# Kernel optimization log

Measured on AMD Instinct MI355X. Metric: run time of the kernel, lower is better.

## Reference

```python
import jax, jax.numpy as jnp
import numpy as np

NUM_STATES = 4096
SEQ_LEN = 4096


def setup_inputs() -> dict:
    key = jax.random.key(0)
    k1, k2, k3, k4 = jax.random.split(key, 4)
    state_dist = jax.random.uniform(k1, (NUM_STATES,), dtype=jnp.float32)
    input_seq = jax.random.randint(k2, (SEQ_LEN,), 0, 2, dtype=jnp.int64)
    T = jax.random.normal(k3, (NUM_STATES, 2, NUM_STATES), dtype=jnp.float32) * 0.1
    O = jax.random.normal(k4, (NUM_STATES, 2, 4), dtype=jnp.float32) * 0.1
    return {"state_dist": state_dist, "input_seq": input_seq, "T": T, "O": O}


def reference(state_dist, input_seq, T, O):
    # Softmax over last dim -> row-stochastic transition / emission matrices.
    Tm = jax.nn.softmax(T, axis=-1)  # [N, 2, N]
    Om = jax.nn.softmax(O, axis=-1)  # [N, 2, 4]

    def step(state, sym):
        # (O[:, sym, :] * state[:, None]).sum(0) == state @ O[:, sym, :]
        O_s = jnp.take(Om, sym, axis=1)          # [N, 4]
        T_s = jnp.take(Tm, sym, axis=1)          # [N, N]
        out_prob = state @ O_s                    # [4]
        new_state = state @ T_s                   # [N]
        return new_state, out_prob

    _, outputs = jax.lax.scan(step, state_dist, input_seq)
    return outputs  # [L, 4]
```

## Files before the change

### kernel.cpp

```cpp
#include <hip/hip_runtime.h>
#include <hip/hip_fp16.h>

#define N 4096
#define L 4096
#define NPART 16
#define NJB 32
#define CPB 128
#define RPB 256

#define NN ((size_t)N * (size_t)N)
#define SLOT ((size_t)N * 4)
#define VTN ((size_t)NPART * N)

#define ASU(p, v) __hip_atomic_store((p), (v), __ATOMIC_RELAXED, __HIP_MEMORY_SCOPE_AGENT)
#define ALU(p)    __hip_atomic_load((p), __ATOMIC_RELAXED, __HIP_MEMORY_SCOPE_AGENT)

typedef _Float16 f16x8 __attribute__((ext_vector_type(8)));
typedef float f32x4 __attribute__((ext_vector_type(4)));

__global__ __launch_bounds__(256) void init_kernel(const float* __restrict__ sd,
                                                   unsigned long long* __restrict__ vt,
                                                   float* __restrict__ rcacc,
                                                   float* __restrict__ out) {
    int g = blockIdx.x * 256 + threadIdx.x;
    if (g < L * 4) out[g] = 0.0f;
    if (g < (int)(3 * VTN)) {
        float val = (g < N) ? sd[g] : 0.0f;
        ASU(&vt[g], (unsigned long long)__float_as_uint(val));
    }
    if (g < 16 * N) rcacc[g] = 0.0f;
}

__global__ __launch_bounds__(256) void build_desc_kernel(const int* __restrict__ seq32,
                                                         unsigned char* __restrict__ midx,
                                                         int mode) {
    __shared__ int any_odd;
    if (threadIdx.x == 0) any_odd = 0;
    __syncthreads();
    int acc = 0;
    for (int i = threadIdx.x; i < L / 2; i += 256) acc |= seq32[2 * i + 1];
    if (acc) any_odd = 1;
    __syncthreads();
    const int is64 = (any_odd == 0);
#define SYM(t) ((is64 ? seq32[2 * (t)] : seq32[(t)]) & 1)
    if (mode == 2) {
        for (int k = threadIdx.x; k < L / 4; k += 256)
            midx[k] = (unsigned char)(SYM(4 * k) * 8 + SYM(4 * k + 1) * 4 +
                                      SYM(4 * k + 2) * 2 + SYM(4 * k + 3));
    } else if (mode == 1) {
        for (int k = threadIdx.x; k < L / 2; k += 256)
            midx[k] = (unsigned char)(SYM(2 * k) * 2 + SYM(2 * k + 1));
    } else {
        for (int t = threadIdx.x; t < L; t += 256)
            midx[t] = (unsigned char)SYM(t);
    }
#undef SYM
}

__global__ __launch_bounds__(256) void softmax_T_kernel(const float* __restrict__ T,
                                                        unsigned short* __restrict__ Tm,
                                                        float* __restrict__ rowc) {
    int row = blockIdx.x;
    int i = row >> 1, s = row & 1;
    const float* src = T + (size_t)row * N;
    unsigned short* dst = Tm + ((size_t)s << 24) + ((size_t)i << 12);
    int tid = threadIdx.x;

    float vals[16];
    float mx = -1e30f;
#pragma unroll
    for (int k = 0; k < 16; k++) {
        vals[k] = src[tid + (k << 8)];
        mx = fmaxf(mx, vals[k]);
    }
#pragma unroll
    for (int o = 32; o > 0; o >>= 1) mx = fmaxf(mx, __shfl_xor(mx, o));
    __shared__ float red[4];
    int wid = tid >> 6;
    if ((tid & 63) == 0) red[wid] = mx;
    __syncthreads();
    mx = fmaxf(fmaxf(red[0], red[1]), fmaxf(red[2], red[3]));
    __syncthreads();

    float sum = 0.0f;
#pragma unroll
    for (int k = 0; k < 16; k++) {
        vals[k] = __expf(vals[k] - mx);
        sum += vals[k];
    }
#pragma unroll
    for (int o = 32; o > 0; o >>= 1) sum += __shfl_xor(sum, o);
    if ((tid & 63) == 0) red[wid] = sum;
    __syncthreads();
    sum = red[0] + red[1] + red[2] + red[3];
    __syncthreads();
    float inv = 1.0f / sum;

    float qs = 0.0f;
#pragma unroll
    for (int k = 0; k < 16; k++) {
        __half h = __float2half_rn(vals[k] * inv);
        dst[tid + (k << 8)] = __half_as_ushort(h);
        qs += __half2float(h);
    }
#pragma unroll
    for (int o = 32; o > 0; o >>= 1) qs += __shfl_xor(qs, o);
    if ((tid & 63) == 0) red[wid] = qs;
    __syncthreads();
    if (tid == 0) {
        float q = red[0] + red[1] + red[2] + red[3];
        rowc[(size_t)s * N + i] = 1.0f / q;
    }
}

__global__ __launch_bounds__(256) void softmax_O_kernel(const float* __restrict__ O,
                                                        float* __restrict__ OW) {
    int r = blockIdx.x * 256 + threadIdx.x;
    if (r < 2 * N) {
        float4 x = *(const float4*)(O + (size_t)r * 4);
        float mx = fmaxf(fmaxf(x.x, x.y), fmaxf(x.z, x.w));
        float e0 = __expf(x.x - mx), e1 = __expf(x.y - mx);
        float e2 = __expf(x.z - mx), e3 = __expf(x.w - mx);
        float inv = 1.0f / (e0 + e1 + e2 + e3);
        int i = r >> 1, s = r & 1;
        *(float4*)(OW + (size_t)s * SLOT + (size_t)i * 4) =
            make_float4(e0 * inv, e1 * inv, e2 * inv, e3 * inv);
    }
}

template <int Q8OUT>
__global__ __launch_bounds__(256) void gemm_kernel(const unsigned short* __restrict__ Abase,
                                                   const unsigned short* __restrict__ Bbase,
                                                   void* __restrict__ Cbase,
                                                   float* __restrict__ rcacc,
                                                   int ash, int bmask) {
    int bid = blockIdx.x;
    int pair = bid >> 10;
    int tile = bid & 1023;
    int i0 = (tile >> 5) << 7;
    int j0 = (tile & 31) << 7;
    const unsigned short* A = Abase + (size_t)(pair >> ash) * NN;
    const unsigned short* B = Bbase + (size_t)(pair & bmask) * NN;

    __shared__ _Float16 Asd[128][40];
    __shared__ unsigned int Btw[128][20];

    const int tid = threadIdx.x;
    const int w = tid >> 6, ln = tid & 63;
    const int wrow = (w >> 1) << 6, wcol = (w & 1) << 6;
    const int q = ln >> 4, l15 = ln & 15;

    const int ar = tid >> 1, ah = tid & 1;
    const int bk2 = tid & 15, bng = tid >> 4;

    f32x4 acc[4][4] = {};

    for (int k0 = 0; k0 < N; k0 += 32) {
        const uint4* ga = (const uint4*)(A + (size_t)(i0 + ar) * N + k0 + ah * 16);
        uint4 a0 = ga[0], a1 = ga[1];
        *(uint4*)&Asd[ar][ah * 16] = a0;
        *(uint4*)&Asd[ar][ah * 16 + 8] = a1;
        const unsigned short* gb0 = B + (size_t)(k0 + 2 * bk2) * N + j0 + bng * 8;
        uint4 b0 = *(const uint4*)gb0;
        uint4 b1 = *(const uint4*)(gb0 + N);
        const unsigned short* e0 = (const unsigned short*)&b0;
        const unsigned short* e1 = (const unsigned short*)&b1;
#pragma unroll
        for (int jj = 0; jj < 8; jj++)
            Btw[bng * 8 + jj][bk2] = (unsigned)e0[jj] | ((unsigned)e1[jj] << 16);
        __syncthreads();

        f16x8 af[4], bf[4];
#pragma unroll
        for (int ti = 0; ti < 4; ti++)
            af[ti] = *(const f16x8*)&Asd[wrow + ti * 16 + l15][q * 8];
#pragma unroll
        for (int tj = 0; tj < 4; tj++)
            bf[tj] = *(const f16x8*)&Btw[wcol + tj * 16 + l15][q * 4];
#pragma unroll
        for (int ti = 0; ti < 4; ti++)
#pragma unroll
            for (int tj = 0; tj < 4; tj++)
                acc[ti][tj] = __builtin_amdgcn_mfma_f32_16x16x32_f16(
                    af[ti], bf[tj], acc[ti][tj], 0, 0, 0);
        __syncthreads();
    }

    if (Q8OUT == 0) {
        unsigned short* Pm = (unsigned short*)Cbase + (size_t)pair * NN;
#pragma unroll
        for (int ti = 0; ti < 4; ti++)
#pragma unroll
            for (int tj = 0; tj < 4; tj++)
#pragma unroll
                for (int reg = 0; reg < 4; reg++) {
                    int row = i0 + wrow + ti * 16 + q * 4 + reg;
                    int col = j0 + wcol + tj * 16 + l15;
                    Pm[(size_t)row * N + col] =
                        __half_as_ushort(__float2half_rn(acc[ti][tj][reg]));
                }
    } else {
        unsigned char* Pm8 = (unsigned char*)Cbase + (size_t)pair * NN;
        float* rcrow = rcacc + (size_t)pair * N;
#pragma unroll
        for (int ti = 0; ti < 4; ti++)
#pragma unroll
            for (int reg = 0; reg < 4; reg++) {
                int row = i0 + wrow + ti * 16 + q * 4 + reg;
                float rs = 0.0f;
#pragma unroll
                for (int tj = 0; tj < 4; tj++) {
                    float f = acc[ti][tj][reg] * 16384.0f;
                    unsigned hb = __half_as_ushort(__float2half_rn(f));
                    unsigned r = hb + 0x3Fu + ((hb >> 7) & 1u);
                    int qv = (int)(r >> 7) - 64;
                    qv = qv < 8 ? 8 : (qv > 0x7E ? 0x7E : qv);
                    unsigned short db = (unsigned short)((qv + 64) << 7);
                    rs += __half2float(*reinterpret_cast<const __half*>(&db));
                    Pm8[(size_t)row * N + j0 + wcol + tj * 16 + l15] = (unsigned char)qv;
                }
                rs += __shfl_xor(rs, 1); rs += __shfl_xor(rs, 2);
                rs += __shfl_xor(rs, 4); rs += __shfl_xor(rs, 8);
                if (l15 == 0) atomicAdd(&rcrow[row], rs);
            }
    }
}

__global__ __launch_bounds__(256) void rcinv_kernel(float* __restrict__ rc) {
    int g = blockIdx.x * 256 + threadIdx.x;
    if (g < 16 * N) rc[g] = 1.0f / rc[g];
}

__global__ __launch_bounds__(256) void rowsum_kernel(const unsigned short* __restrict__ P,
                                                     float* __restrict__ rc) {
    int b = blockIdx.x;
    const unsigned short* row = P + (size_t)b * N;
    int tid = threadIdx.x;
    const uint4* rp = (const uint4*)row + tid * 2;
    uint4 w0 = rp[0], w1 = rp[1];
    const __half* h0 = (const __half*)&w0;
    const __half* h1 = (const __half*)&w1;
    float s = 0.0f;
#pragma unroll
    for (int j = 0; j < 8; j++) s += __half2float(h0[j]) + __half2float(h1[j]);
#pragma unroll
    for (int o = 32; o > 0; o >>= 1) s += __shfl_xor(s, o);
    __shared__ float red[4];
    if ((tid & 63) == 0) red[tid >> 6] = s;
    __syncthreads();
    if (tid == 0) rc[b] = 1.0f / (red[0] + red[1] + red[2] + red[3]);
}

__global__ __launch_bounds__(256) void proj_kernel(const unsigned short* __restrict__ Tm,
                                                   const unsigned short* __restrict__ P,
                                                   const float* __restrict__ rowc,
                                                   const float* __restrict__ rowc2,
                                                   float* __restrict__ OW, int phase) {
    int bid = blockIdx.x;
    int s = bid >> 12, i = bid & 4095;
    const unsigned short* M; const float* rc; const float* Q; float* dst;
    if (phase == 1) {
        if (s < 4) { M = Tm + (size_t)(s >> 1) * NN; rc = rowc + (size_t)(s >> 1) * N;
                     Q = OW + (size_t)(s & 1) * SLOT; dst = OW + (size_t)(2 + s) * SLOT; }
        else { int q = s - 4; M = P + (size_t)(q >> 1) * NN; rc = rowc2 + (size_t)(q >> 1) * N;
               Q = OW + (size_t)(q & 1) * SLOT; dst = OW + (size_t)(6 + q) * SLOT; }
    } else {
        int q = s; M = P + (size_t)(q >> 2) * NN; rc = rowc2 + (size_t)(q >> 2) * N;
        Q = OW + (size_t)(2 + (q & 3)) * SLOT; dst = OW + (size_t)(14 + q) * SLOT;
    }
    const unsigned short* row = M + (size_t)i * N;
    int tid = threadIdx.x;
    const uint4* rp = (const uint4*)row + tid * 2;
    uint4 w0 = rp[0], w1 = rp[1];
    const __half* h0 = (const __half*)&w0;
    const __half* h1 = (const __half*)&w1;
    int j0 = tid * 16;
    float ac[4] = {};
#pragma unroll
    for (int j = 0; j < 8; j++) {
        float tv = __half2float(h0[j]);
        float4 o = *(const float4*)(Q + (size_t)(j0 + j) * 4);
        ac[0] += tv * o.x; ac[1] += tv * o.y; ac[2] += tv * o.z; ac[3] += tv * o.w;
        float tv1 = __half2float(h1[j]);
        float4 o1 = *(const float4*)(Q + (size_t)(j0 + 8 + j) * 4);
        ac[0] += tv1 * o1.x; ac[1] += tv1 * o1.y; ac[2] += tv1 * o1.z; ac[3] += tv1 * o1.w;
    }
#pragma unroll
    for (int e = 0; e < 4; e++)
#pragma unroll
        for (int o = 32; o > 0; o >>= 1) ac[e] += __shfl_xor(ac[e], o);
    __shared__ float red[4][4];
    if ((tid & 63) == 0)
#pragma unroll
        for (int e = 0; e < 4; e++) red[tid >> 6][e] = ac[e];
    __syncthreads();
    if (tid < 4)
        dst[(size_t)i * 4 + tid] =
            (red[0][tid] + red[1][tid] + red[2][tid] + red[3][tid]) * rc[i];
}

__device__ __forceinline__ float2 d8x2(unsigned b0, unsigned b1) {
    unsigned pk = ((b0 + 64u) << 7) | ((b1 + 64u) << 23);
    return __half22float2(*reinterpret_cast<__half2*>(&pk));
}

#define SPIN_SUM(vinp, kk, accv)                                               \
    {                                                                          \
        unsigned long long uv[16];                                             \
        _Pragma("unroll")                                                      \
        for (int p = 0; p < 16; p++) uv[p] = ALU((vinp) + p * N);              \
        unsigned miss = 0;                                                     \
        _Pragma("unroll")                                                      \
        for (int p = 0; p < 16; p++)                                           \
            if ((unsigned)(uv[p] >> 32) != (kk)) miss |= 1u << p;              \
        while (__builtin_expect(miss != 0, 0)) {                               \
            _Pragma("unroll")                                                  \
            for (int p = 0; p < 16; p++)                                       \
                if (miss & (1u << p)) {                                        \
                    unsigned long long t = ALU((vinp) + p * N);                \
                    if ((unsigned)(t >> 32) == (kk)) { uv[p] = t; miss &= ~(1u << p); } \
                }                                                              \
        }                                                                      \
        _Pragma("unroll")                                                      \
        for (int p = 0; p < 16; p++) accv += __uint_as_float((unsigned)uv[p]); \
    }

__global__ __launch_bounds__(256, 2) void scan8_kernel(const unsigned char* __restrict__ Q8,
                                                       const float* __restrict__ rc,
                                                       const float* __restrict__ OW,
                                                       const unsigned char* __restrict__ midx,
                                                       unsigned long long* __restrict__ vt,
                                                       float* __restrict__ out,
                                                       int S, int OPS) {
    const int tid = threadIdx.x;
    const int jb = blockIdx.x & 31;
    const int ic = blockIdx.x >> 5;
    const int i0 = ic * RPB;
    const int j0 = jb * CPB;

    __shared__ unsigned char mt8[2][RPB][CPB];
    __shared__ float v[RPB];
    __shared__ float vc[RPB];
    __shared__ float colacc[CPB];

    const int cg = tid & 15;
    const int rg = tid >> 4;

    const int w4 = tid >> 6;
    const int ln = tid & 63;
    const size_t goff8 = (size_t)(i0 + (ln >> 3)) * N + j0 + (ln & 7) * 16;

#define STAGE8(Mb, dst)                                                         \
    _Pragma("unroll")                                                           \
    for (int t = 0; t < 8; t++) {                                               \
        const int row0 = w4 * 64 + t * 8;                                       \
        __builtin_amdgcn_global_load_lds(                                       \
            (const __attribute__((address_space(1))) unsigned int*)((Mb) + goff8 + (size_t)row0 * N), \
            (__attribute__((address_space(3))) unsigned int*)((dst) + (size_t)row0 * CPB),            \
            16, 0, 0);                                                          \
    }

    int mcur = (int)midx[0];
    int mnxt = (S > 1) ? (int)midx[1] : 0;
    float rc_cur = rc[(size_t)mcur * N + i0 + tid];
    float rc_nxt = (S > 1) ? rc[(size_t)mnxt * N + i0 + tid] : 0.0f;
    STAGE8(Q8 + (size_t)mcur * NN, &mt8[0][0][0]);

    for (int k = 0; k < S; k++) {
        const int m = mcur;
        const unsigned long long* vinp = vt + (size_t)(k % 3) * VTN + (i0 + tid);
        unsigned long long* voutp = vt + (size_t)((k + 1) % 3) * VTN + (size_t)ic * N + j0;
        const unsigned char* mtc = &mt8[k & 1][0][0];

        float accv = 0.0f;
        SPIN_SUM(vinp, (unsigned)k, accv);
        v[tid] = accv;
        vc[tid] = accv * rc_cur;
        if (tid < CPB) colacc[tid] = 0.0f;

        if (k + 1 < S) {
            STAGE8(Q8 + (size_t)mnxt * NN, &mt8[(k + 1) & 1][0][0]);
            asm volatile("s_waitcnt vmcnt(8) lgkmcnt(0)" ::: "memory");
        } else {
            asm volatile("s_waitcnt vmcnt(0) lgkmcnt(0)" ::: "memory");
        }
        __builtin_amdgcn_s_barrier();
        __builtin_amdgcn_sched_barrier(0);

        float a[8];
#pragma unroll
        for (int e = 0; e < 8; e++) a[e] = 0.0f;
#pragma unroll
        for (int r = 0; r < 16; r++) {
            uint2 w = *(const uint2*)(mtc + (size_t)(rg * 16 + r) * CPB + cg * 8);
            float vi = vc[rg * 16 + r];
            float2 f0 = d8x2(w.x & 0xFF, (w.x >> 8) & 0xFF);
            float2 f1 = d8x2((w.x >> 16) & 0xFF, w.x >> 24);
            float2 f2 = d8x2(w.y & 0xFF, (w.y >> 8) & 0xFF);
            float2 f3 = d8x2((w.y >> 16) & 0xFF, w.y >> 24);
            a[0] += vi * f0.x; a[1] += vi * f0.y;
            a[2] += vi * f1.x; a[3] += vi * f1.y;
            a[4] += vi * f2.x; a[5] += vi * f2.y;
            a[6] += vi * f3.x; a[7] += vi * f3.y;
        }
#pragma unroll
        for (int e = 0; e < 8; e++) atomicAdd(&colacc[cg * 8 + e], a[e]);

        if (jb < OPS) {
            int slot;
            if (OPS == 4) slot = (jb == 0) ? (m >> 3) : (jb == 1) ? 2 + (m >> 2)
                               : (jb == 2) ? 6 + (m >> 1) : 14 + m;
            else if (OPS == 2) slot = (jb == 0) ? (m >> 1) : 2 + m;
            else slot = m;
            const float* pr = OW + (size_t)slot * SLOT;
            int r = tid >> 2, c = tid & 3;
            float p = v[r]       * pr[(size_t)(i0 + r) * 4 + c]
                    + v[r + 64]  * pr[(size_t)(i0 + r + 64) * 4 + c]
                    + v[r + 128] * pr[(size_t)(i0 + r + 128) * 4 + c]
                    + v[r + 192] * pr[(size_t)(i0 + r + 192) * 4 + c];
            p += __shfl_down(p, 32); p += __shfl_down(p, 16);
            p += __shfl_down(p, 8);  p += __shfl_down(p, 4);
            if ((tid & 63) < 4) atomicAdd(&out[(k * OPS + jb) * 4 + (tid & 3)], p);
        }

        asm volatile("s_waitcnt lgkmcnt(0)" ::: "memory");
        __builtin_amdgcn_s_barrier();
        __builtin_amdgcn_sched_barrier(0);

        if (tid < CPB) {
            unsigned long long pk = ((unsigned long long)(unsigned)(k + 1) << 32)
                                  | (unsigned long long)__float_as_uint(colacc[tid]);
            ASU(&voutp[tid], pk);
        }
        mcur = mnxt; rc_cur = rc_nxt;
        if (k + 2 < S) {
            mnxt = (int)midx[k + 2];
            rc_nxt = rc[(size_t)mnxt * N + i0 + tid];
        }
    }
#undef STAGE8
}

__global__ __launch_bounds__(256, 2) void scan16_kernel(const unsigned short* __restrict__ Mbase,
                                                        const float* __restrict__ rc,
                                                        const float* __restrict__ OW,
                                                        const unsigned char* __restrict__ midx,
                                                        unsigned long long* __restrict__ vt,
                                                        float* __restrict__ out,
                                                        int S, int OPS) {
    const int tid = threadIdx.x;
    const int jb = blockIdx.x & 31;
    const int ic = blockIdx.x >> 5;
    const int i0 = ic * RPB;
    const int j0 = jb * CPB;

    __shared__ unsigned short mt[RPB][CPB];
    __shared__ float v[RPB];
    __shared__ float vc[RPB];
    __shared__ float colacc[CPB];

    const int cg = tid & 15;
    const int rg = tid >> 4;

    const int w4 = tid >> 6;
    const int ln = tid & 63;
    const size_t goff = (size_t)(i0 + (ln >> 4)) * N + j0 + (ln & 15) * 8;

    int mcur = (int)midx[0];
    int mnxt = (S > 1) ? (int)midx[1] : 0;
    float rc_cur = rc[(size_t)mcur * N + i0 + tid];
    float rc_nxt = (S > 1) ? rc[(size_t)mnxt * N + i0 + tid] : 0.0f;
    {
        const unsigned short* Mb = Mbase + (size_t)mcur * NN;
#pragma unroll
        for (int t = 0; t < 16; t++) {
            const int row0 = w4 * 64 + t * 4;
            __builtin_amdgcn_global_load_lds(
                (const __attribute__((address_space(1))) unsigned int*)(Mb + goff + (size_t)row0 * N),
                (__attribute__((address_space(3))) unsigned int*)(&mt[row0][0]),
                16, 0, 0);
        }
    }

    for (int k = 0; k < S; k++) {
        const int m = mcur;
        const unsigned long long* vinp = vt + (size_t)(k % 3) * VTN + (i0 + tid);
        unsigned long long* voutp = vt + (size_t)((k + 1) % 3) * VTN + (size_t)ic * N + j0;

        float accv = 0.0f;
        SPIN_SUM(vinp, (unsigned)k, accv);
        v[tid] = accv;
        vc[tid] = accv * rc_cur;
        if (tid < CPB) colacc[tid] = 0.0f;
        __syncthreads();

        float a[8];
#pragma unroll
        for (int e = 0; e < 8; e++) a[e] = 0.0f;
#pragma unroll
        for (int r = 0; r < 16; r++) {
            uint4 w = *(const uint4*)&mt[rg * 16 + r][cg * 8];
            float vi = vc[rg * 16 + r];
            float2 f0 = __half22float2(*(__half2*)&w.x);
            float2 f1 = __half22float2(*(__half2*)&w.y);
            float2 f2 = __half22float2(*(__half2*)&w.z);
            float2 f3 = __half22float2(*(__half2*)&w.w);
            a[0] += vi * f0.x; a[1] += vi * f0.y;
            a[2] += vi * f1.x; a[3] += vi * f1.y;
            a[4] += vi * f2.x; a[5] += vi * f2.y;
            a[6] += vi * f3.x; a[7] += vi * f3.y;
        }
#pragma unroll
        for (int e = 0; e < 8; e++) atomicAdd(&colacc[cg * 8 + e], a[e]);

        if (jb < OPS) {
            int slot;
            if (OPS == 4) slot = (jb == 0) ? (m >> 3) : (jb == 1) ? 2 + (m >> 2)
                               : (jb == 2) ? 6 + (m >> 1) : 14 + m;
            else if (OPS == 2) slot = (jb == 0) ? (m >> 1) : 2 + m;
            else slot = m;
            const float* pr = OW + (size_t)slot * SLOT;
            int r = tid >> 2, c = tid & 3;
            float p = v[r]       * pr[(size_t)(i0 + r) * 4 + c]
                    + v[r + 64]  * pr[(size_t)(i0 + r + 64) * 4 + c]
                    + v[r + 128] * pr[(size_t)(i0 + r + 128) * 4 + c]
                    + v[r + 192] * pr[(size_t)(i0 + r + 192) * 4 + c];
            p += __shfl_down(p, 32); p += __shfl_down(p, 16);
            p += __shfl_down(p, 8);  p += __shfl_down(p, 4);
            if ((tid & 63) < 4) atomicAdd(&out[(k * OPS + jb) * 4 + (tid & 3)], p);
        }
        __syncthreads();

        if (tid < CPB) {
            unsigned long long pk = ((unsigned long long)(unsigned)(k + 1) << 32)
                                  | (unsigned long long)__float_as_uint(colacc[tid]);
            ASU(&voutp[tid], pk);
        }
        if (k + 1 < S) {
            const unsigned short* Mb = Mbase + (size_t)mnxt * NN;
#pragma unroll
            for (int t = 0; t < 16; t++) {
                const int row0 = w4 * 64 + t * 4;
                __builtin_amdgcn_global_load_lds(
                    (const __attribute__((address_space(1))) unsigned int*)(Mb + goff + (size_t)row0 * N),
                    (__attribute__((address_space(3))) unsigned int*)(&mt[row0][0]),
                    16, 0, 0);
            }
        }
        mcur = mnxt; rc_cur = rc_nxt;
        if (k + 2 < S) {
            mnxt = (int)midx[k + 2];
            rc_nxt = rc[(size_t)mnxt * N + i0 + tid];
        }
    }
}

extern "C" void kernel_launch(void* const* d_in, const int* in_sizes, int n_in,
                              void* d_out, int out_size, void* d_ws, size_t ws_size,
                              hipStream_t stream) {
    const float* sd  = (const float*)d_in[0];
    const int*   seq = (const int*)d_in[1];
    const float* T   = (const float*)d_in[2];
    const float* O   = (const float*)d_in[3];
    float* out = (float*)d_out;

    const size_t TM_SZ = 2 * NN * 2;
    const size_t P_SZ  = 4 * NN * 2;
    const size_t Q8_SZ = 16 * NN;
    const size_t AUX_SZ = 0x400000;

    int mode = (ws_size >= TM_SZ + P_SZ + Q8_SZ + AUX_SZ) ? 3
             : (ws_size >= TM_SZ + P_SZ + AUX_SZ) ? 1 : 0;

    char* ws = (char*)d_ws;
    unsigned short* Tm = (unsigned short*)ws;
    unsigned short* P  = (unsigned short*)(ws + TM_SZ);
    unsigned char*  Q8 = (unsigned char*)(ws + TM_SZ + P_SZ);
    char* aux = ws + (mode == 3 ? TM_SZ + P_SZ + Q8_SZ
                    : mode == 1 ? TM_SZ + P_SZ : TM_SZ);
    float* rowc   = (float*)(aux);
    float* rowc2  = (float*)(aux + 0x8000);
    float* rowc4  = (float*)(aux + 0x18000);
    float* OW     = (float*)(aux + 0x58000);
    unsigned long long* vt = (unsigned long long*)(aux + 0x258000);
    unsigned char* midx = (unsigned char*)(aux + 0x3D8000);

    hipLaunchKernelGGL(init_kernel, dim3(1536), dim3(256), 0, stream, sd, vt, rowc4, out);
    hipLaunchKernelGGL(build_desc_kernel, dim3(1), dim3(256), 0, stream, seq, midx,
                       mode == 3 ? 2 : mode);
    hipLaunchKernelGGL(softmax_T_kernel, dim3(2 * N), dim3(256), 0, stream, T, Tm, rowc);
    hipLaunchKernelGGL(softmax_O_kernel, dim3(32), dim3(256), 0, stream, O, OW);

    if (mode == 3) {
        hipLaunchKernelGGL(HIP_KERNEL_NAME(gemm_kernel<0>), dim3(4 * 1024), dim3(256), 0, stream,
                           Tm, Tm, (void*)P, rowc4, 1, 1);
        hipLaunchKernelGGL(rowsum_kernel, dim3(4 * N), dim3(256), 0, stream, P, rowc2);
        hipLaunchKernelGGL(HIP_KERNEL_NAME(gemm_kernel<1>), dim3(16 * 1024), dim3(256), 0, stream,
                           P, P, (void*)Q8, rowc4, 2, 3);
        hipLaunchKernelGGL(rcinv_kernel, dim3(256), dim3(256), 0, stream, rowc4);
        hipLaunchKernelGGL(proj_kernel, dim3(12 * N), dim3(256), 0, stream, Tm, P, rowc, rowc2, OW, 1);
        hipLaunchKernelGGL(proj_kernel, dim3(16 * N), dim3(256), 0, stream, Tm, P, rowc, rowc2, OW, 2);
        hipLaunchKernelGGL(scan8_kernel, dim3(512), dim3(256), 0, stream,
                           Q8, rowc4, OW, midx, vt, out, L / 4, 4);
    } else if (mode == 1) {
        hipLaunchKernelGGL(HIP_KERNEL_NAME(gemm_kernel<0>), dim3(4 * 1024), dim3(256), 0, stream,
                           Tm, Tm, (void*)P, rowc4, 1, 1);
        hipLaunchKernelGGL(rowsum_kernel, dim3(4 * N), dim3(256), 0, stream, P, rowc2);
        hipLaunchKernelGGL(proj_kernel, dim3(4 * N), dim3(256), 0, stream, Tm, P, rowc, rowc2, OW, 1);
        hipLaunchKernelGGL(scan16_kernel, dim3(512), dim3(256), 0, stream,
                           P, rowc2, OW, midx, vt, out, L / 2, 2);
    } else {
        hipLaunchKernelGGL(scan16_kernel, dim3(512), dim3(256), 0, stream,
                           Tm, rowc, OW, midx, vt, out, L, 1);
    }
}
```

Measured before the change: 15.18 ms.

## Gate scan steps on per-producer ready flags and publish results earlier

Adds a ready-flag array. Each block publishes a step counter after writing its partial column sums, and consumer blocks wait on the 32 producer flags with sleeping polls before reading the packed vector values. The partial-vector store and flag publish are moved ahead of the output-probability computation, so downstream blocks can start the next step sooner. s_sleep is also added to the miss-retry loop to reduce memory pressure from spinning. The cost is an extra barrier and flag traffic per step, and possible added latency from the sleeps.

```diff
diff --git a/kernel.cpp b/kernel.cpp
--- a/kernel.cpp
+++ b/kernel.cpp
@@ -21,6 +21,7 @@
 __global__ __launch_bounds__(256) void init_kernel(const float* __restrict__ sd,
                                                    unsigned long long* __restrict__ vt,
                                                    float* __restrict__ rcacc,
+                                                   unsigned* __restrict__ ready,
                                                    float* __restrict__ out) {
     int g = blockIdx.x * 256 + threadIdx.x;
     if (g < L * 4) out[g] = 0.0f;
@@ -29,6 +30,7 @@
         ASU(&vt[g], (unsigned long long)__float_as_uint(val));
     }
     if (g < 16 * N) rcacc[g] = 0.0f;
+    if (g < NPART * 64) ASU(&ready[g], 0u);
 }
 
 __global__ __launch_bounds__(256) void build_desc_kernel(const int* __restrict__ seq32,
@@ -314,6 +316,7 @@
         for (int p = 0; p < 16; p++)                                           \
             if ((unsigned)(uv[p] >> 32) != (kk)) miss |= 1u << p;              \
         while (__builtin_expect(miss != 0, 0)) {                               \
+            __builtin_amdgcn_s_sleep(1);                                       \
             _Pragma("unroll")                                                  \
             for (int p = 0; p < 16; p++)                                       \
                 if (miss & (1u << p)) {                                        \
@@ -330,6 +333,7 @@
                                                        const float* __restrict__ OW,
                                                        const unsigned char* __restrict__ midx,
                                                        unsigned long long* __restrict__ vt,
+                                                       unsigned* __restrict__ ready,
                                                        float* __restrict__ out,
                                                        int S, int OPS) {
     const int tid = threadIdx.x;
@@ -349,6 +353,9 @@
     const int w4 = tid >> 6;
     const int ln = tid & 63;
     const size_t goff8 = (size_t)(i0 + (ln >> 3)) * N + j0 + (ln & 7) * 16;
+
+    unsigned* wait_flags = &ready[ic * 64];
+    unsigned* my_flag    = &ready[(jb >> 1) * 64 + ic * 2 + (jb & 1)];
 
 #define STAGE8(Mb, dst)                                                         \
     _Pragma("unroll")                                                           \
@@ -371,6 +378,13 @@
         const unsigned long long* vinp = vt + (size_t)(k % 3) * VTN + (i0 + tid);
         unsigned long long* voutp = vt + (size_t)((k + 1) % 3) * VTN + (size_t)ic * N + j0;
         const unsigned char* mtc = &mt8[k & 1][0][0];
+
+        if (tid < 32) {
+            while (ALU(&wait_flags[tid]) < (unsigned)k) __builtin_amdgcn_s_sleep(2);
+        }
+        asm volatile("" ::: "memory");
+        __builtin_amdgcn_s_barrier();
+        asm volatile("" ::: "memory");
 
         float accv = 0.0f;
         SPIN_SUM(vinp, (unsigned)k, accv);
@@ -405,6 +419,17 @@
         }
 #pragma unroll
         for (int e = 0; e < 8; e++) atomicAdd(&colacc[cg * 8 + e], a[e]);
+
+        asm volatile("s_waitcnt lgkmcnt(0)" ::: "memory");
+        __builtin_amdgcn_s_barrier();
+        __builtin_amdgcn_sched_barrier(0);
+
+        if (tid < CPB) {
+            unsigned long long pk = ((unsigned long long)(unsigned)(k + 1) << 32)
+                                  | (unsigned long long)__float_as_uint(colacc[tid]);
+            ASU(&voutp[tid], pk);
+        }
+        if (tid == 0) ASU(my_flag, (unsigned)(k + 1));
 
         if (jb < OPS) {
             int slot;
@@ -423,15 +448,6 @@
             if ((tid & 63) < 4) atomicAdd(&out[(k * OPS + jb) * 4 + (tid & 3)], p);
         }
 
-        asm volatile("s_waitcnt lgkmcnt(0)" ::: "memory");
-        __builtin_amdgcn_s_barrier();
-        __builtin_amdgcn_sched_barrier(0);
-
-        if (tid < CPB) {
-            unsigned long long pk = ((unsigned long long)(unsigned)(k + 1) << 32)
-                                  | (unsigned long long)__float_as_uint(colacc[tid]);
-            ASU(&voutp[tid], pk);
-        }
         mcur = mnxt; rc_cur = rc_nxt;
         if (k + 2 < S) {
             mnxt = (int)midx[k + 2];
@@ -446,6 +462,7 @@
                                                         const float* __restrict__ OW,
                                                         const unsigned char* __restrict__ midx,
                                                         unsigned long long* __restrict__ vt,
+                                                        unsigned* __restrict__ ready,
                                                         float* __restrict__ out,
                                                         int S, int OPS) {
     const int tid = threadIdx.x;
@@ -466,6 +483,9 @@
     const int ln = tid & 63;
     const size_t goff = (size_t)(i0 + (ln >> 4)) * N + j0 + (ln & 15) * 8;
 
+    unsigned* wait_flags = &ready[ic * 64];
+    unsigned* my_flag    = &ready[(jb >> 1) * 64 + ic * 2 + (jb & 1)];
+
     int mcur = (int)midx[0];
     int mnxt = (S > 1) ? (int)midx[1] : 0;
     float rc_cur = rc[(size_t)mcur * N + i0 + tid];
@@ -486,6 +506,13 @@
         const int m = mcur;
         const unsigned long long* vinp = vt + (size_t)(k % 3) * VTN + (i0 + tid);
         unsigned long long* voutp = vt + (size_t)((k + 1) % 3) * VTN + (size_t)ic * N + j0;
+
+        if (tid < 32) {
+            while (ALU(&wait_flags[tid]) < (unsigned)k) __builtin_amdgcn_s_sleep(2);
+        }
+        asm volatile("" ::: "memory");
+        __builtin_amdgcn_s_barrier();
+        asm volatile("" ::: "memory");
 
         float accv = 0.0f;
         SPIN_SUM(vinp, (unsigned)k, accv);
@@ -512,6 +539,14 @@
         }
 #pragma unroll
         for (int e = 0; e < 8; e++) atomicAdd(&colacc[cg * 8 + e], a[e]);
+        __syncthreads();
+
+        if (tid < CPB) {
+            unsigned long long pk = ((unsigned long long)(unsigned)(k + 1) << 32)
+                                  | (unsigned long long)__float_as_uint(colacc[tid]);
+            ASU(&voutp[tid], pk);
+        }
+        if (tid == 0) ASU(my_flag, (unsigned)(k + 1));
 
         if (jb < OPS) {
             int slot;
@@ -529,13 +564,7 @@
             p += __shfl_down(p, 8);  p += __shfl_down(p, 4);
             if ((tid & 63) < 4) atomicAdd(&out[(k * OPS + jb) * 4 + (tid & 3)], p);
         }
-        __syncthreads();
-
-        if (tid < CPB) {
-            unsigned long long pk = ((unsigned long long)(unsigned)(k + 1) << 32)
-                                  | (unsigned long long)__float_as_uint(colacc[tid]);
-            ASU(&voutp[tid], pk);
-        }
+
         if (k + 1 < S) {
             const unsigned short* Mb = Mbase + (size_t)mnxt * NN;
 #pragma unroll
@@ -584,8 +613,9 @@
     float* OW     = (float*)(aux + 0x58000);
     unsigned long long* vt = (unsigned long long*)(aux + 0x258000);
     unsigned char* midx = (unsigned char*)(aux + 0x3D8000);
-
-    hipLaunchKernelGGL(init_kernel, dim3(1536), dim3(256), 0, stream, sd, vt, rowc4, out);
+    unsigned* ready = (unsigned*)(aux + 0x3D9000);
+
+    hipLaunchKernelGGL(init_kernel, dim3(1536), dim3(256), 0, stream, sd, vt, rowc4, ready, out);
     hipLaunchKernelGGL(build_desc_kernel, dim3(1), dim3(256), 0, stream, seq, midx,
                        mode == 3 ? 2 : mode);
     hipLaunchKernelGGL(softmax_T_kernel, dim3(2 * N), dim3(256), 0, stream, T, Tm, rowc);
@@ -601,16 +631,16 @@
         hipLaunchKernelGGL(proj_kernel, dim3(12 * N), dim3(256), 0, stream, Tm, P, rowc, rowc2, OW, 1);
         hipLaunchKernelGGL(proj_kernel, dim3(16 * N), dim3(256), 0, stream, Tm, P, rowc, rowc2, OW, 2);
         hipLaunchKernelGGL(scan8_kernel, dim3(512), dim3(256), 0, stream,
-                           Q8, rowc4, OW, midx, vt, out, L / 4, 4);
+                           Q8, rowc4, OW, midx, vt, ready, out, L / 4, 4);
     } else if (mode == 1) {
         hipLaunchKernelGGL(HIP_KERNEL_NAME(gemm_kernel<0>), dim3(4 * 1024), dim3(256), 0, stream,
                            Tm, Tm, (void*)P, rowc4, 1, 1);
         hipLaunchKernelGGL(rowsum_kernel, dim3(4 * N), dim3(256), 0, stream, P, rowc2);
         hipLaunchKernelGGL(proj_kernel, dim3(4 * N), dim3(256), 0, stream, Tm, P, rowc, rowc2, OW, 1);
         hipLaunchKernelGGL(scan16_kernel, dim3(512), dim3(256), 0, stream,
-                           P, rowc2, OW, midx, vt, out, L / 2, 2);
+                           P, rowc2, OW, midx, vt, ready, out, L / 2, 2);
     } else {
         hipLaunchKernelGGL(scan16_kernel, dim3(512), dim3(256), 0, stream,
-                           Tm, rowc, OW, midx, vt, out, L, 1);
-    }
-}
+                           Tm, rowc, OW, midx, vt, ready, out, L, 1);
+    }
+}
```

Result: slower. 16.00 ms (+5.4%).

## Use direct global-to-LDS loads with XOR swizzle, K=64 tiles, and XCD-aware block remap

Applied to the files above, without the earlier changes.

The GEMM kernel's K-step doubles from 32 to 64, which halves the number of barriers per tile. The A tile is loaded with global_load_lds straight into an XOR-swizzled shared-memory layout, skipping the round trip through registers and avoiding bank conflicts. Block IDs are remapped so consecutive tiles land on the same XCD, which should improve L2 reuse. In exchange, shared memory use and register pressure both rise.

```diff
diff --git a/kernel.cpp b/kernel.cpp
--- a/kernel.cpp
+++ b/kernel.cpp
@@ -134,7 +134,9 @@
                                                    void* __restrict__ Cbase,
                                                    float* __restrict__ rcacc,
                                                    int ash, int bmask) {
-    int bid = blockIdx.x;
+    const int nwg = gridDim.x;
+    int bid0 = blockIdx.x;
+    int bid = (bid0 & 7) * (nwg >> 3) + (bid0 >> 3);
     int pair = bid >> 10;
     int tile = bid & 1023;
     int i0 = (tile >> 5) << 7;
@@ -142,47 +144,67 @@
     const unsigned short* A = Abase + (size_t)(pair >> ash) * NN;
     const unsigned short* B = Bbase + (size_t)(pair & bmask) * NN;
 
-    __shared__ _Float16 Asd[128][40];
-    __shared__ unsigned int Btw[128][20];
+    __shared__ _Float16 Asd[128 * 64];
+    __shared__ unsigned int Btw[128][36];
 
     const int tid = threadIdx.x;
     const int w = tid >> 6, ln = tid & 63;
     const int wrow = (w >> 1) << 6, wcol = (w & 1) << 6;
     const int q = ln >> 4, l15 = ln & 15;
 
-    const int ar = tid >> 1, ah = tid & 1;
-    const int bk2 = tid & 15, bng = tid >> 4;
+    const int kp = tid & 31, cgB = tid >> 5;
+
+    const int gA = (ln & 7) ^ (ln >> 3);
 
     f32x4 acc[4][4] = {};
 
-    for (int k0 = 0; k0 < N; k0 += 32) {
-        const uint4* ga = (const uint4*)(A + (size_t)(i0 + ar) * N + k0 + ah * 16);
-        uint4 a0 = ga[0], a1 = ga[1];
-        *(uint4*)&Asd[ar][ah * 16] = a0;
-        *(uint4*)&Asd[ar][ah * 16 + 8] = a1;
-        const unsigned short* gb0 = B + (size_t)(k0 + 2 * bk2) * N + j0 + bng * 8;
-        uint4 b0 = *(const uint4*)gb0;
-        uint4 b1 = *(const uint4*)(gb0 + N);
-        const unsigned short* e0 = (const unsigned short*)&b0;
-        const unsigned short* e1 = (const unsigned short*)&b1;
+    for (int k0 = 0; k0 < N; k0 += 64) {
+#pragma unroll
+        for (int t = 0; t < 4; t++) {
+            const int rbase = w * 32 + t * 8;
+            const int r = rbase + (ln >> 3);
+            __builtin_amdgcn_global_load_lds(
+                (const __attribute__((address_space(1))) unsigned int*)
+                    (A + (size_t)(i0 + r) * N + k0 + gA * 8),
+                (__attribute__((address_space(3))) unsigned int*)(Asd + rbase * 64),
+                16, 0, 0);
+        }
+        const unsigned short* gb0 = B + (size_t)(k0 + 2 * kp) * N + j0 + cgB * 16;
+        uint4 b0  = *(const uint4*)gb0;
+        uint4 b0h = *(const uint4*)(gb0 + 8);
+        uint4 b1  = *(const uint4*)(gb0 + N);
+        uint4 b1h = *(const uint4*)(gb0 + N + 8);
+        const unsigned short* e0  = (const unsigned short*)&b0;
+        const unsigned short* e1  = (const unsigned short*)&b1;
+        const unsigned short* e0h = (const unsigned short*)&b0h;
+        const unsigned short* e1h = (const unsigned short*)&b1h;
 #pragma unroll
         for (int jj = 0; jj < 8; jj++)
-            Btw[bng * 8 + jj][bk2] = (unsigned)e0[jj] | ((unsigned)e1[jj] << 16);
+            Btw[cgB * 16 + jj][kp] = (unsigned)e0[jj] | ((unsigned)e1[jj] << 16);
+#pragma unroll
+        for (int jj = 0; jj < 8; jj++)
+            Btw[cgB * 16 + 8 + jj][kp] = (unsigned)e0h[jj] | ((unsigned)e1h[jj] << 16);
         __syncthreads();
 
-        f16x8 af[4], bf[4];
-#pragma unroll
-        for (int ti = 0; ti < 4; ti++)
-            af[ti] = *(const f16x8*)&Asd[wrow + ti * 16 + l15][q * 8];
-#pragma unroll
-        for (int tj = 0; tj < 4; tj++)
-            bf[tj] = *(const f16x8*)&Btw[wcol + tj * 16 + l15][q * 4];
-#pragma unroll
-        for (int ti = 0; ti < 4; ti++)
+#pragma unroll
+        for (int kk = 0; kk < 2; kk++) {
+            f16x8 af[4], bf[4];
+#pragma unroll
+            for (int ti = 0; ti < 4; ti++) {
+                const int R = wrow + ti * 16 + l15;
+                const int G = (kk * 4 + q) ^ (l15 & 7);
+                af[ti] = *(const f16x8*)(Asd + R * 64 + G * 8);
+            }
 #pragma unroll
             for (int tj = 0; tj < 4; tj++)
-                acc[ti][tj] = __builtin_amdgcn_mfma_f32_16x16x32_f16(
-                    af[ti], bf[tj], acc[ti][tj], 0, 0, 0);
+                bf[tj] = *(const f16x8*)&Btw[wcol + tj * 16 + l15][kk * 16 + q * 4];
+#pragma unroll
+            for (int ti = 0; ti < 4; ti++)
+#pragma unroll
+                for (int tj = 0; tj < 4; tj++)
+                    acc[ti][tj] = __builtin_amdgcn_mfma_f32_16x16x32_f16(
+                        af[ti], bf[tj], acc[ti][tj], 0, 0, 0);
+        }
         __syncthreads();
     }
 
```

Result: no change. 15.36 ms (+1.2%).
